# Performance work log

Hardware: AMD Instinct MI355X
Metric: run time of the kernel (lower is better)

## Reference

```python
import jax, jax.numpy as jnp
import numpy as np

N = 1024      # params.input_dim (f1 is a square [N, N] similarity matrix)
TOPK = 16     # params.topk
B = 64        # hardcoded batch in the original reshape
W = 2 * N // B  # spatial width after reshape


def setup_inputs() -> dict:
    key = jax.random.key(0)
    k1, k2, k3 = jax.random.split(key, 3)
    f1 = jax.random.normal(k1, (N, N), dtype=jnp.float32)
    # Conv2d(in=N, out=N, kernel=(TOPK, 1)) weights, kaiming-ish scale
    conv_w = jax.random.normal(k2, (N, N, TOPK, 1), dtype=jnp.float32) * 0.01
    conv_b = jax.random.normal(k3, (N,), dtype=jnp.float32) * 0.01
    return {"f1": f1, "conv_w": conv_w, "conv_b": conv_b}


def reference(f1, conv_w, conv_b):
    # i = topk indices along last dim (largest, sorted) -> [N, TOPK]
    _, idx = jax.lax.top_k(f1, TOPK)
    # pos = f1[i]: gather rows of f1 by the topk column indices -> [N, TOPK, N]
    pos = f1[idx]
    # repeat_interleave(TOPK, dim=0).reshape(N, TOPK, -1) == each row tiled TOPK times
    rep = jnp.broadcast_to(f1[:, None, :], (N, TOPK, N))
    # cat on dim=2 -> [N, TOPK, 2N]; reshape to NCHW [B, N, TOPK, W]
    out = jnp.concatenate([rep, pos], axis=2).reshape(B, N, TOPK, W)
    # Conv2d kernel (TOPK, 1), VALID padding collapses H -> 1: [B, N, 1, W]
    y = jax.lax.conv_general_dilated(
        out, conv_w, window_strides=(1, 1), padding='VALID',
        dimension_numbers=('NCHW', 'OIHW', 'NCHW'))
    y = y + conv_b[None, :, None, None]
    return jax.nn.relu(y).reshape(N, -1)  # [N, B*W] = [N, 2N]
```

## Files before the change

kernel.cpp:

```cpp
#include <hip/hip_runtime.h>
#include <stdint.h>


#define NDIM 1024
#define TK   16
#define KPOS 8192
#define KREP 512
#define NCOL 2048

typedef unsigned short u16;
typedef uint32_t u32;
typedef u16   u16x8  __attribute__((ext_vector_type(8)));
typedef __bf16 bf16x8 __attribute__((ext_vector_type(8)));
typedef float  f32x4  __attribute__((ext_vector_type(4)));

__device__ __forceinline__ u16 f2bf(float x) {
    union { float f; unsigned u; } v; v.f = x;
    unsigned r = 0x7FFFu + ((v.u >> 16) & 1u);
    return (u16)((v.u + r) >> 16);
}

__device__ __forceinline__ void load_lds_16B(const u16* g, u16* l) {
    __builtin_amdgcn_global_load_lds(
        (__attribute__((address_space(1))) void*)(uintptr_t)g,
        (__attribute__((address_space(3))) void*)(unsigned)(uintptr_t)l,
        16, 0, 0);
}

#define PREP_TOPK 256
#define PREP_ZERO 512
#define PREP_W    1024
#define PREP_F1T  256

__global__ __launch_bounds__(256) void prep_kernel(const float* __restrict__ f1,
                                                   const float* __restrict__ W,
                                                   int* __restrict__ idx,
                                                   u16* __restrict__ Wb,
                                                   u16* __restrict__ W1b,
                                                   u16* __restrict__ f1t,
                                                   float* __restrict__ out) {
    const int bid = blockIdx.x;
    const int t = threadIdx.x;
    if (bid < PREP_TOPK) {
        const int lane = t & 63;
        const int row  = bid * 4 + (t >> 6);
        float v[16];
        const float* src = f1 + row * NDIM + lane;
        #pragma unroll
        for (int j = 0; j < 16; ++j) v[j] = src[j * 64];
        for (int sel = 0; sel < TK; ++sel) {
            float best = -3.402823466e38f; int bg = 0x7fffffff;
            #pragma unroll
            for (int j = 0; j < 16; ++j)
                if (v[j] > best) { best = v[j]; bg = j * 64 + lane; }
            #pragma unroll
            for (int s = 1; s < 64; s <<= 1) {
                float ov = __shfl_xor(best, s);
                int   og = __shfl_xor(bg, s);
                if (ov > best || (ov == best && og < bg)) { best = ov; bg = og; }
            }
            if (lane == sel) idx[row * TK + sel] = bg;
            #pragma unroll
            for (int j = 0; j < 16; ++j)
                if (bg == j * 64 + lane) v[j] = -3.402823466e38f;
        }
    } else if (bid < PREP_TOPK + PREP_ZERO) {
        const int zb = bid - PREP_TOPK;
        f32x4 z = {0.f, 0.f, 0.f, 0.f};
        float* p = out + (size_t)zb * 4096 + t * 16;
        #pragma unroll
        for (int j = 0; j < 4; ++j) *(f32x4*)(p + j * 4) = z;
    } else if (bid < PREP_TOPK + PREP_ZERO + PREP_W) {
        const int o = bid - PREP_TOPK - PREP_ZERO;
        const float* wrow = W + (size_t)o * 16384;
        u16* wbrow = Wb + (size_t)o * KPOS;
        #pragma unroll
        for (int j = 0; j < 4; ++j) {
            const int v = j * 2048 + t * 8;
            const int u = ((v >> 5) << 6) + 32 + (v & 31);
            float4 a = *(const float4*)(wrow + u);
            float4 b = *(const float4*)(wrow + u + 4);
            u16x8 ov;
            ov[0] = f2bf(a.x); ov[1] = f2bf(a.y); ov[2] = f2bf(a.z); ov[3] = f2bf(a.w);
            ov[4] = f2bf(b.x); ov[5] = f2bf(b.y); ov[6] = f2bf(b.z); ov[7] = f2bf(b.w);
            *(u16x8*)(wbrow + v) = ov;
        }
        #pragma unroll
        for (int h = 0; h < 2; ++h) {
            const int kr = h * 256 + t;
            const int nl = kr >> 5, e = kr & 31;
            const float* base = wrow + nl * 1024 + e;
            float s = 0.f;
            #pragma unroll
            for (int tt = 0; tt < 16; ++tt) s += base[tt * 64];
            W1b[o * KREP + kr] = f2bf(s);
        }
    } else {
        const int gb = bid - PREP_TOPK - PREP_ZERO - PREP_W;
        const int unit = t >> 5;
        const int w = t & 31;
        const int rq = gb * 8 + unit;
        const int row = rq >> 1, q = rq & 1;
        const float* src = f1 + row * NDIM + q * 512;
        const int swp = ((w >> 2) & 1) * 8;
        u16 tmp[16];
        #pragma unroll
        for (int kh = 0; kh < 16; ++kh)
            tmp[kh ^ swp] = f2bf(src[kh * 32 + w]);
        u16* dst = f1t + ((size_t)row * 2 + q) * 512 + w * 16;
        *(u16x8*)(dst)     = *(u16x8*)(tmp);
        *(u16x8*)(dst + 8) = *(u16x8*)(tmp + 8);
    }
}

#define BM 128
#define BN 128
#define BK 64
#define KITERS 17

__global__ __launch_bounds__(256, 3) void gemm_kernel(const u16* __restrict__ Ap,
                                                      const u16* __restrict__ A1,
                                                      const u16* __restrict__ f1t,
                                                      const int* __restrict__ idx,
                                                      float* __restrict__ out) {
    __shared__ __align__(16) u16 As[BM * BK];
    __shared__ __align__(16) u16 Bs[2][16 * 512];
    __shared__ __align__(8) int idxO[272];
    const int f = blockIdx.x;
    const int m = f & 7;
    const int g = f >> 3;
    const int n = g & 15;
    const int z = g >> 4;
    const int t    = threadIdx.x;
    const int lane = t & 63;
    const int wave = t >> 6;
    const int wm   = (wave >> 1) * 64;
    const int wn   = (wave & 1) * 64;
    const int quad = lane >> 4;
    const int l16  = lane & 15;
    const int sw   = l16 & 7;
    const int o0 = m * BM;
    const int n0 = n * BN;
    const int nb0 = n * 4;

    {
        const int j = t >> 2, bl = t & 3;
        const int ip = z * 64 + j;
        const int nl = ip >> 5, tt = (ip >> 1) & 15, q = ip & 1;
        const int row = idx[((nb0 + bl) * 16 + nl) * TK + tt];
        idxO[j * 4 + bl] = ((row << 1) + q) << 9;
        if (t < 16) {
            const int ci = t >> 2, bl2 = t & 3;
            const int ur = z * 4 + ci;
            const int rrow = (nb0 + bl2) * 16 + (ur >> 1);
            idxO[(64 + ci) * 4 + bl2] = ((rrow << 1) + (ur & 1)) << 9;
        }
    }

    f32x4 acc[4][4] = {};

    const int rA = t >> 3;
    const int c8 = t & 7;
    const int csw = (c8 ^ (rA & 7)) * 8;
    const u16* gApos = Ap + (size_t)(o0 + rA) * KPOS + z * 1024 + csw;
    const u16* gArep = A1 + (size_t)(o0 + rA) * KREP + z * 64 + csw;

    auto stageA = [&](int it) {
        u16* lA = As + t * 8;
        if (it < 16) {
            const int k0 = it * BK;
            #pragma unroll
            for (int c = 0; c < 4; ++c)
                load_lds_16B(gApos + (size_t)(c * 32) * KPOS + k0, lA + c * 2048);
        } else {
            #pragma unroll
            for (int c = 0; c < 4; ++c)
                load_lds_16B(gArep + (size_t)(c * 32) * KREP, lA + c * 2048);
        }
    };

    auto stageB = [&](int it, int nb) {
        const int u0 = (it < 16) ? (it * 4 + wave) : (64 + wave);
        #pragma unroll
        for (int bl = 0; bl < 4; ++bl)
            load_lds_16B(f1t + idxO[u0 * 4 + bl] + lane * 8,
                         Bs[nb] + (wave * 4 + bl) * 512);
    };

    __syncthreads();
    stageB(0, 0);

    for (int it = 0; it < KITERS; ++it) {
        const int cur = it & 1;
        stageA(it);
        if (it + 1 < KITERS) stageB(it + 1, 1 - cur);
        __syncthreads();

        #pragma unroll
        for (int ks = 0; ks < 2; ++ks) {
            bf16x8 af[4], bfr[4];
            #pragma unroll
            for (int mt = 0; mt < 4; ++mt) {
                u16x8 bits = *(const u16x8*)(As + (wm + mt * 16 + l16) * BK
                                                + (((ks * 4 + quad) ^ sw) * 8));
                af[mt] = __builtin_bit_cast(bf16x8, bits);
            }
            const int ci2 = ks * 2 + (quad >> 1);
            const int qh  = quad & 1;
            #pragma unroll
            for (int nt = 0; nt < 4; ++nt) {
                const int nn = wn + nt * 16 + l16;
                const int blocf = nn >> 5, w = nn & 31;
                u16x8 bits = *(const u16x8*)(Bs[cur] + (ci2 * 4 + blocf) * 512 + w * 16
                                                + ((qh ^ ((w >> 2) & 1)) * 8));
                bfr[nt] = __builtin_bit_cast(bf16x8, bits);
            }
            #pragma unroll
            for (int mt = 0; mt < 4; ++mt)
                #pragma unroll
                for (int nt = 0; nt < 4; ++nt)
                    acc[mt][nt] = __builtin_amdgcn_mfma_f32_16x16x32_bf16(
                        af[mt], bfr[nt], acc[mt][nt], 0, 0, 0);
        }
        __syncthreads();
    }

    #pragma unroll
    for (int nt = 0; nt < 4; ++nt) {
        const int nn = n0 + wn + nt * 16 + l16;
        const int bb = nn >> 5, w = nn & 31;
        #pragma unroll
        for (int mt = 0; mt < 4; ++mt) {
            #pragma unroll
            for (int r = 0; r < 4; ++r) {
                const int o = o0 + wm + mt * 16 + quad * 4 + r;
                unsafeAtomicAdd(out + (size_t)(bb * 16 + (o >> 6)) * 2048
                                    + (o & 63) * 32 + w,
                                acc[mt][nt][r]);
            }
        }
    }
}

__global__ __launch_bounds__(256) void finalize_kernel(float* __restrict__ out,
                                                       const float* __restrict__ bias) {
    const int tid = blockIdx.x * 256 + threadIdx.x;
    const int f = tid * 4;
    const int o = ((f >> 11) & 15) * 64 + ((f & 2047) >> 5);
    const float bv = bias[o];
    float4 x = *(float4*)(out + f);
    x.x = fmaxf(x.x + bv, 0.f);
    x.y = fmaxf(x.y + bv, 0.f);
    x.z = fmaxf(x.z + bv, 0.f);
    x.w = fmaxf(x.w + bv, 0.f);
    *(float4*)(out + f) = x;
}

extern "C" void kernel_launch(void* const* d_in, const int* in_sizes, int n_in,
                              void* d_out, int out_size, void* d_ws, size_t ws_size,
                              hipStream_t stream) {
    const float* f1   = (const float*)d_in[0];
    const float* Wc   = (const float*)d_in[1];
    const float* bias = (const float*)d_in[2];
    float* out = (float*)d_out;

    int* idx = (int*)d_ws;
    u16* Wb  = (u16*)((char*)d_ws + 65536);
    u16* W1b = (u16*)((char*)d_ws + 16842752);
    u16* f1t = (u16*)((char*)d_ws + 17891328);

    prep_kernel<<<PREP_TOPK + PREP_ZERO + PREP_W + PREP_F1T,
                  256, 0, stream>>>(f1, Wc, idx, Wb, W1b, f1t, out);
    gemm_kernel<<<1024, 256, 0, stream>>>(Wb, W1b, f1t, idx, out);
    finalize_kernel<<<(NDIM * NCOL) / (4 * 256), 256, 0, stream>>>(out, bias);
}
```

Before: 184.2 us.

## Prefetch next A tile into double-buffered LDS and stage gathered B via registers

Restructures the main loop so the next A tile goes into a second LDS buffer asynchronously while the current tile is computed. The gathered B rows are now loaded into registers and written to a single LDS buffer after compute, replacing the double-buffered async global-to-LDS path. Row indices are cached raw in LDS and offsets are computed per iteration. This aims to overlap global latency with MFMA work and cut sync stalls, at the cost of more registers and an extra barrier. The raw s_barrier before writeB relies on the LDS reads in compute having completed.

```diff
diff --git a/kernel.cpp b/kernel.cpp
--- a/kernel.cpp
+++ b/kernel.cpp
@@ -123,9 +123,9 @@
                                                       const u16* __restrict__ f1t,
                                                       const int* __restrict__ idx,
                                                       float* __restrict__ out) {
-    __shared__ __align__(16) u16 As[BM * BK];
-    __shared__ __align__(16) u16 Bs[2][16 * 512];
-    __shared__ __align__(8) int idxO[272];
+    __shared__ __align__(16) u16 As[2][BM * BK];
+    __shared__ __align__(16) u16 Bs[16 * 512];
+    __shared__ int idxL[128];
     const int f = blockIdx.x;
     const int m = f & 7;
     const int g = f >> 3;
@@ -143,18 +143,9 @@
     const int n0 = n * BN;
     const int nb0 = n * 4;
 
-    {
-        const int j = t >> 2, bl = t & 3;
-        const int ip = z * 64 + j;
-        const int nl = ip >> 5, tt = (ip >> 1) & 15, q = ip & 1;
-        const int row = idx[((nb0 + bl) * 16 + nl) * TK + tt];
-        idxO[j * 4 + bl] = ((row << 1) + q) << 9;
-        if (t < 16) {
-            const int ci = t >> 2, bl2 = t & 3;
-            const int ur = z * 4 + ci;
-            const int rrow = (nb0 + bl2) * 16 + (ur >> 1);
-            idxO[(64 + ci) * 4 + bl2] = ((rrow << 1) + (ur & 1)) << 9;
-        }
+    if (t < 128) {
+        const int bl = t >> 5, nlz = (t >> 4) & 1, tt = t & 15;
+        idxL[t] = idx[((nb0 + bl) * 16 + z * 2 + nlz) * TK + tt];
     }
 
     f32x4 acc[4][4] = {};
@@ -165,8 +156,8 @@
     const u16* gApos = Ap + (size_t)(o0 + rA) * KPOS + z * 1024 + csw;
     const u16* gArep = A1 + (size_t)(o0 + rA) * KREP + z * 64 + csw;
 
-    auto stageA = [&](int it) {
-        u16* lA = As + t * 8;
+    auto stageA = [&](int it, int nb) {
+        u16* lA = As[nb] + t * 8;
         if (it < 16) {
             const int k0 = it * BK;
             #pragma unroll
@@ -179,29 +170,42 @@
         }
     };
 
-    auto stageB = [&](int it, int nb) {
-        const int u0 = (it < 16) ? (it * 4 + wave) : (64 + wave);
+    u16x8 breg[4];
+    auto loadB = [&](int it) {
+        int rows[4], qp;
+        if (it < 16) {
+            const int ip = z * 64 + it * 4 + wave;
+            qp = ip & 1;
+            const int nlz = (ip >> 5) & 1, tt = (ip >> 1) & 15;
+            #pragma unroll
+            for (int bl = 0; bl < 4; ++bl)
+                rows[bl] = idxL[bl * 32 + nlz * 16 + tt];
+        } else {
+            const int ip = z * 4 + wave;
+            qp = ip & 1;
+            const int nlr = ip >> 1;
+            #pragma unroll
+            for (int bl = 0; bl < 4; ++bl)
+                rows[bl] = (nb0 + bl) * 16 + nlr;
+        }
         #pragma unroll
         for (int bl = 0; bl < 4; ++bl)
-            load_lds_16B(f1t + idxO[u0 * 4 + bl] + lane * 8,
-                         Bs[nb] + (wave * 4 + bl) * 512);
-    };
-
-    __syncthreads();
-    stageB(0, 0);
-
-    for (int it = 0; it < KITERS; ++it) {
-        const int cur = it & 1;
-        stageA(it);
-        if (it + 1 < KITERS) stageB(it + 1, 1 - cur);
-        __syncthreads();
-
+            breg[bl] = *(const u16x8*)(f1t + ((size_t)rows[bl] * 2 + qp) * 512
+                                           + lane * 8);
+    };
+    auto writeB = [&]() {
+        #pragma unroll
+        for (int bl = 0; bl < 4; ++bl)
+            *(u16x8*)(Bs + (wave * 4 + bl) * 512 + lane * 8) = breg[bl];
+    };
+
+    auto compute = [&](const u16* AsX) {
         #pragma unroll
         for (int ks = 0; ks < 2; ++ks) {
             bf16x8 af[4], bfr[4];
             #pragma unroll
             for (int mt = 0; mt < 4; ++mt) {
-                u16x8 bits = *(const u16x8*)(As + (wm + mt * 16 + l16) * BK
+                u16x8 bits = *(const u16x8*)(AsX + (wm + mt * 16 + l16) * BK
                                                 + (((ks * 4 + quad) ^ sw) * 8));
                 af[mt] = __builtin_bit_cast(bf16x8, bits);
             }
@@ -211,7 +215,7 @@
             for (int nt = 0; nt < 4; ++nt) {
                 const int nn = wn + nt * 16 + l16;
                 const int blocf = nn >> 5, w = nn & 31;
-                u16x8 bits = *(const u16x8*)(Bs[cur] + (ci2 * 4 + blocf) * 512 + w * 16
+                u16x8 bits = *(const u16x8*)(Bs + (ci2 * 4 + blocf) * 512 + w * 16
                                                 + ((qh ^ ((w >> 2) & 1)) * 8));
                 bfr[nt] = __builtin_bit_cast(bf16x8, bits);
             }
@@ -222,7 +226,26 @@
                     acc[mt][nt] = __builtin_amdgcn_mfma_f32_16x16x32_bf16(
                         af[mt], bfr[nt], acc[mt][nt], 0, 0, 0);
         }
-        __syncthreads();
+    };
+
+    __syncthreads();
+    loadB(0);
+    stageA(0, 0);
+    writeB();
+    __syncthreads();
+
+    for (int it = 0; it < KITERS; ++it) {
+        const int cur = it & 1;
+        if (it + 1 < KITERS) {
+            loadB(it + 1);
+            stageA(it + 1, cur ^ 1);
+        }
+        compute(As[cur]);
+        if (it + 1 < KITERS) {
+            asm volatile("s_barrier" ::: "memory");
+            writeB();
+            __syncthreads();
+        }
     }
 
     #pragma unroll
```

Result: faster. 180.1 us (-2.2%).
